# Kernel optimization log

Hardware: AMD Instinct MI355X
Metric: run time of the kernel (lower is better)

## Reference

```python
import jax, jax.numpy as jnp
import numpy as np

DIM = 128
GROUPS = [1, 2, 2, 3]


def setup_inputs() -> dict:
    key = jax.random.key(0)
    ks = jax.random.split(key, 8)
    c = DIM
    def p(k, shape, scale=0.02):
        return jax.random.normal(k, shape, dtype=jnp.float32) * scale
    return {
        "x": jax.random.normal(ks[0], (8, c, 128, 128), dtype=jnp.float32),
        "temperature": jnp.ones((4, 1, 1), dtype=jnp.float32),
        "w_qkv": p(ks[1], (3 * c, c)),            # Conv2d(dim, 3*dim, 1), bias=False
        "w_dw": p(ks[2], (3 * c, 1, 3, 3)),        # depthwise 3x3, groups=3*dim
        "w_proj": p(ks[3], (c, c)),                # Conv2d(dim, dim, 1), bias=False
        "w_gate": p(ks[4], (c, c)),                # Intra gatingConv (Conv1d k=1)
        "b_gate": jnp.zeros((c,), jnp.float32),
        "w_down": p(ks[5], (c // 2, c)),           # Intra down
        "b_down": jnp.zeros((c // 2,), jnp.float32),
        "w_up": p(ks[6], (c, c // 2)),             # Intra up
        "b_up": jnp.zeros((c,), jnp.float32),
    }


def _group_sizes(c):
    total = sum(GROUPS)
    sizes = [int(r / total * c) for r in GROUPS]
    sizes[-1] += c - sum(sizes)
    return sizes


def _forward(x, temperature, w_qkv, w_dw, w_proj, w_gate, b_gate,
             w_down, b_down, w_up, b_up):
    b, c, h, w = x.shape
    L = h * w
    # qkv = dwconv3x3(conv1x1(x))
    qkv = jnp.einsum('bchw,oc->bohw', x, w_qkv)
    qkv = jax.lax.conv_general_dilated(
        qkv, w_dw, (1, 1), 'SAME', feature_group_count=3 * c,
        dimension_numbers=('NCHW', 'OIHW', 'NCHW'))
    q, k, v = jnp.split(qkv.reshape(b, 3 * c, L), 3, axis=1)
    # ReGroup: sort channels by mean q activation (descending), split into groups
    channel_mean = q.mean(axis=(0, 2))            # (c,)
    idx = jnp.argsort(-channel_mean)
    q, k, v = q[:, idx], k[:, idx], v[:, idx]
    sizes = _group_sizes(c)
    outs, caches, cache_means = [], [], []
    start = 0
    for i, g in enumerate(sizes):
        qg = q[:, start:start + g]
        kg = k[:, start:start + g]
        vg = v[:, start:start + g]
        start += g
        qn = qg / jnp.maximum(jnp.linalg.norm(qg, axis=-1, keepdims=True), 1e-12)
        kn = kg / jnp.maximum(jnp.linalg.norm(kg, axis=-1, keepdims=True), 1e-12)
        attn = jax.nn.softmax(
            jnp.einsum('bcl,bdl->bcd', qn, kn) * temperature[i, 0, 0], axis=-1)
        outs.append(jnp.einsum('bcd,bdl->bcl', attn, vg))   # (b, g, L)
        tc = jax.lax.stop_gradient(qn + kn)                 # detached cache
        caches.append(tc)
        # per-group mean over L, channel-tiled/padded to c (for cache update)
        gm = tc.mean(axis=-1)                               # (b, g)
        rep = max(1, c // g)
        gm = jnp.tile(gm, (1, rep))
        gm = gm[:, :c] if gm.shape[1] >= c else jnp.pad(gm, ((0, 0), (0, c - gm.shape[1])))
        cache_means.append(gm)
    out_all = jnp.concatenate(outs, axis=1)       # (b, c, L)
    tmp_caches = jnp.concatenate(caches, axis=1)  # (b, c, L)
    # CalculateCurrentLayerCache: bilinear upsample of (1,1) map == broadcast
    s = int(L ** 0.5 + 0.9999)
    acc = sum(cache_means) / float(len(cache_means))        # (b, c)
    qv_cache = jnp.broadcast_to((acc * 0.9)[:, :, None, None], (b, c, s, s))
    # Intra cache modulation: gated = gelu(conv(x1+x2)) * (x1+x2); up(down(gated))
    sxy = out_all + tmp_caches
    gating = jax.nn.gelu(jnp.einsum('bcl,oc->bol', sxy, w_gate) + b_gate[:, None],
                         approximate=False)
    gated = gating * sxy
    mod = jnp.einsum('bcl,oc->bol', gated, w_down) + b_down[:, None]
    mod = jnp.einsum('bcl,oc->bol', mod, w_up) + b_up[:, None]
    out_all = mod + out_all
    out_all = jnp.einsum('bchw,oc->bohw', out_all.reshape(b, c, h, w), w_proj)
    return out_all, qv_cache


def reference(x, temperature, w_qkv, w_dw, w_proj, w_gate, b_gate,
              w_down, b_down, w_up, b_up):
    return _forward(x, temperature, w_qkv, w_dw, w_proj, w_gate, b_gate,
                    w_down, b_down, w_up, b_up)
```

## Files before the change

kernel.cpp:

```cpp
#include <hip/hip_runtime.h>
#include <math.h>

#define B_ 8
#define C_ 128
#define O3_ 384
#define H_ 128
#define W_ 128
#define L_ 16384
#define NS_ 64
#define MAXP_ 2304

typedef float f32x4 __attribute__((ext_vector_type(4)));
typedef short bf16x8 __attribute__((ext_vector_type(8)));

static __device__ __forceinline__ ushort f2bf(float f) {
    uint u = __float_as_uint(f);
    u += 0x7fffu + ((u >> 16) & 1u);
    return (ushort)(u >> 16);
}
static __device__ __forceinline__ float bf2f(ushort h) {
    return __uint_as_float(((uint)h) << 16);
}

__global__ __launch_bounds__(256) void wsplit_k(
    const float* __restrict__ wa, const float* __restrict__ wb,
    const float* __restrict__ wc, const float* __restrict__ wd,
    short* __restrict__ ha, short* __restrict__ la,
    short* __restrict__ hb, short* __restrict__ lb,
    short* __restrict__ hc, short* __restrict__ lc,
    short* __restrict__ hd, short* __restrict__ ld)
{
    const int sel = blockIdx.y;
    const float* w = sel == 0 ? wa : (sel == 1 ? wb : (sel == 2 ? wc : wd));
    short* ph = sel == 0 ? ha : (sel == 1 ? hb : (sel == 2 ? hc : hd));
    short* pl = sel == 0 ? la : (sel == 1 ? lb : (sel == 2 ? lc : ld));
    const int n = sel == 0 ? 49152 : (sel == 1 ? 16384 : 8192);
    const int i = blockIdx.x * 256 + threadIdx.x;
    if (i < n) {
        float v = w[i];
        ushort h = f2bf(v);
        ph[i] = (short)h;
        pl[i] = (short)f2bf(v - bf2f(h));
    }
}

__global__ __launch_bounds__(256) void wsplit1_k(const float* __restrict__ w,
    short* __restrict__ ph, short* __restrict__ pl, int n)
{
    const int i = blockIdx.x * 256 + threadIdx.x;
    if (i < n) {
        float v = w[i];
        ushort h = f2bf(v);
        ph[i] = (short)h;
        pl[i] = (short)f2bf(v - bf2f(h));
    }
}

__global__ __launch_bounds__(256) void transp_k(const float* __restrict__ x,
    short* __restrict__ xhi, short* __restrict__ xlo)
{
    __shared__ float t[128][33];
    const int b = blockIdx.y;
    const int l0 = blockIdx.x * 32;
    const int tid = threadIdx.x;
    {
        const int c = tid >> 1, half = tid & 1;
        const float* src = x + ((size_t)b * C_ + c) * L_ + l0 + half * 16;
#pragma unroll
        for (int u = 0; u < 4; u++) {
            float4 v = *reinterpret_cast<const float4*>(src + u * 4);
            t[c][half * 16 + u * 4 + 0] = v.x;
            t[c][half * 16 + u * 4 + 1] = v.y;
            t[c][half * 16 + u * 4 + 2] = v.z;
            t[c][half * 16 + u * 4 + 3] = v.w;
        }
    }
    __syncthreads();
    {
        const int l = tid >> 3, strip = tid & 7;
        uint hi[8], lo[8];
#pragma unroll
        for (int i = 0; i < 8; i++) {
            float a0 = t[strip * 16 + 2 * i][l], a1 = t[strip * 16 + 2 * i + 1][l];
            ushort h0 = f2bf(a0), h1 = f2bf(a1);
            ushort g0 = f2bf(a0 - bf2f(h0)), g1 = f2bf(a1 - bf2f(h1));
            hi[i] = (uint)h0 | ((uint)h1 << 16);
            lo[i] = (uint)g0 | ((uint)g1 << 16);
        }
        size_t ob = ((size_t)b * L_ + l0 + l) * C_ + strip * 16;
        uint4* ph = reinterpret_cast<uint4*>(xhi + ob);
        uint4* pl = reinterpret_cast<uint4*>(xlo + ob);
        ph[0] = *reinterpret_cast<uint4*>(&hi[0]);
        ph[1] = *reinterpret_cast<uint4*>(&hi[4]);
        pl[0] = *reinterpret_cast<uint4*>(&lo[0]);
        pl[1] = *reinterpret_cast<uint4*>(&lo[4]);
    }
}

template<int KD, int OT, int MODE>
__global__ __launch_bounds__(256) void mgemm_k(
    const short* __restrict__ Whi, const short* __restrict__ Wlo,
    const float* __restrict__ bias,
    const short* __restrict__ Ahi, const short* __restrict__ Alo,
    const float* __restrict__ E0,
    float* __restrict__ Yf, short* __restrict__ Yhi, short* __restrict__ Ylo)
{
    constexpr int WC = OT / 64;
    constexpr int WR = 4 / WC;
    constexpr int LT = WR * 64;
    constexpr int T  = KD / 32;
    constexpr int ABYTES = LT * 64;
    constexpr int BBYTES = OT * KD * 2;
    constexpr int CA = WR;
    constexpr int CB = (OT * KD) / 2048;
    __shared__ __align__(16) char sAh[ABYTES];
    __shared__ __align__(16) char sAl[ABYTES];
    __shared__ __align__(16) char sBh[BBYTES];
    __shared__ __align__(16) char sBl[BBYTES];

    const int tid = threadIdx.x;
    const int lane = tid & 63;
    const int wid = tid >> 6;
    const int wr = wid / WC, wc = wid % WC;
    const int oB = blockIdx.x * OT;
    const int lB = blockIdx.y * LT;
    const int ON = gridDim.x * OT;
    const int b  = blockIdx.z;
    const int ln15 = lane & 15, lg = lane >> 4;
    const int m0A = (ln15 >> 1) & 3;
    const int m0B = ln15 & 3;
    const int m1B = (ln15 >> 2) & (T - 1);

    const size_t abase = ((size_t)b * L_ + lB) * KD;

    {
#pragma unroll
        for (int p = 0; p < CB; p++) {
            const int id = tid + p * 256;
            const int row = id / (KD / 8), cs = id % (KD / 8);
            const int tt = cs >> 2, ks = cs & 3;
            const size_t src = (size_t)(oB + row) * KD + cs * 8;
            const int dst = row * (KD * 2) + ((tt ^ ((row >> 2) & (T - 1))) * 64)
                          + ((ks ^ (row & 3)) << 4);
            *reinterpret_cast<uint4*>(sBh + dst) = *reinterpret_cast<const uint4*>(Whi + src);
            *reinterpret_cast<uint4*>(sBl + dst) = *reinterpret_cast<const uint4*>(Wlo + src);
        }
    }

    uint4 pAh[CA], pAl[CA];
    auto ldgA = [&](int t) {
#pragma unroll
        for (int p = 0; p < CA; p++) {
            const int id = tid + p * 256;
            const int row = id >> 2, s = id & 3;
            const size_t src = abase + (size_t)row * KD + t * 32 + s * 8;
            pAh[p] = *reinterpret_cast<const uint4*>(Ahi + src);
            pAl[p] = *reinterpret_cast<const uint4*>(Alo + src);
        }
    };
    auto stA = [&]() {
#pragma unroll
        for (int p = 0; p < CA; p++) {
            const int id = tid + p * 256;
            const int row = id >> 2, s = id & 3;
            const int dst = row * 64 + ((s ^ ((row >> 1) & 3)) << 4);
            *reinterpret_cast<uint4*>(sAh + dst) = pAh[p];
            *reinterpret_cast<uint4*>(sAl + dst) = pAl[p];
        }
    };

    f32x4 acc[4][4];
#pragma unroll
    for (int m = 0; m < 4; m++)
#pragma unroll
        for (int n = 0; n < 4; n++)
#pragma unroll
            for (int r = 0; r < 4; r++) acc[m][n][r] = 0.f;

    ldgA(0);
    stA();
    __syncthreads();

    for (int t = 0; t < T; t++) {
        bf16x8 Ah[4], Al[4], Bh[4], Bl[4];
#pragma unroll
        for (int m = 0; m < 4; m++) {
            const int row = wr * 64 + m * 16 + ln15;
            const int ab = row * 64 + ((lg ^ m0A) << 4);
            Ah[m] = *reinterpret_cast<const bf16x8*>(sAh + ab);
            Al[m] = *reinterpret_cast<const bf16x8*>(sAl + ab);
        }
#pragma unroll
        for (int n = 0; n < 4; n++) {
            const int row = wc * 64 + n * 16 + ln15;
            const int bb = row * (KD * 2) + ((t ^ m1B) * 64) + ((lg ^ m0B) << 4);
            Bh[n] = *reinterpret_cast<const bf16x8*>(sBh + bb);
            Bl[n] = *reinterpret_cast<const bf16x8*>(sBl + bb);
        }
        __syncthreads();
        if (t + 1 < T) ldgA(t + 1);
#pragma unroll
        for (int n = 0; n < 4; n++)
#pragma unroll
            for (int m = 0; m < 4; m++) {
                acc[m][n] = __builtin_amdgcn_mfma_f32_16x16x32_bf16(Ah[m], Bh[n], acc[m][n], 0, 0, 0);
                acc[m][n] = __builtin_amdgcn_mfma_f32_16x16x32_bf16(Ah[m], Bl[n], acc[m][n], 0, 0, 0);
                acc[m][n] = __builtin_amdgcn_mfma_f32_16x16x32_bf16(Al[m], Bh[n], acc[m][n], 0, 0, 0);
            }
        if (t + 1 < T) { stA(); __syncthreads(); }
    }

#pragma unroll
    for (int m = 0; m < 4; m++) {
        const int l = lB + wr * 64 + m * 16 + lg * 4;
#pragma unroll
        for (int n = 0; n < 4; n++) {
            const int o = oB + wc * 64 + n * 16 + ln15;
            if constexpr (MODE == 4) {
                float4 r4 = {acc[m][n][0], acc[m][n][1], acc[m][n][2], acc[m][n][3]};
                *reinterpret_cast<float4*>(&Yf[((size_t)b * ON + o) * L_ + l]) = r4;
            } else {
                float bv = bias[o];
#pragma unroll
                for (int r = 0; r < 4; r++) {
                    size_t yi = ((size_t)b * L_ + l + r) * ON + o;
                    float a = acc[m][n][r] + bv;
                    if constexpr (MODE == 1) {
                        float sxy = bf2f((ushort)Ahi[yi]) + bf2f((ushort)Alo[yi]);
                        a = 0.5f * a * (1.f + erff(a * 0.70710678118654752f)) * sxy;
                    }
                    if constexpr (MODE == 3) a += E0[yi];
                    ushort h = f2bf(a);
                    ushort g = f2bf(a - bf2f(h));
                    Yhi[yi] = (short)h;
                    Ylo[yi] = (short)g;
                }
            }
        }
    }
}

__global__ __launch_bounds__(256) void dwconv_k(const float* __restrict__ in,
    const float* __restrict__ wdw, float* __restrict__ outp,
    float* __restrict__ sumq, float* __restrict__ sumk,
    float* __restrict__ ssq, float* __restrict__ ssk)
{
    const int ch = blockIdx.x, b = blockIdx.y;
    const int tid = threadIdx.x;
    const int tx = tid & 31, band = tid >> 5;
    const int x0 = tx * 4;
    const int y0 = band * 16;
    const size_t base = ((size_t)b * O3_ + ch) * L_;
    const float* wp = wdw + ch * 9;
    float w0 = wp[0], w1 = wp[1], w2 = wp[2], w3 = wp[3], w4 = wp[4],
          w5 = wp[5], w6 = wp[6], w7 = wp[7], w8 = wp[8];

    float s1 = 0.f, s2 = 0.f;
    float b0[6], b1[6], b2[6];

    auto loadrow = [&](int gy, float* r) {
        if ((unsigned)gy < (unsigned)H_) {
            const float* rp = in + base + (size_t)gy * W_;
            float4 m = *reinterpret_cast<const float4*>(rp + x0);
            r[0] = (x0 > 0) ? rp[x0 - 1] : 0.f;
            r[1] = m.x; r[2] = m.y; r[3] = m.z; r[4] = m.w;
            r[5] = (x0 < W_ - 4) ? rp[x0 + 4] : 0.f;
        } else {
            r[0] = r[1] = r[2] = r[3] = r[4] = r[5] = 0.f;
        }
    };
    auto conv3 = [&](const float* ra, const float* rb, const float* rc, int yy) {
        float o0 = ra[0]*w0 + ra[1]*w1 + ra[2]*w2 + rb[0]*w3 + rb[1]*w4 + rb[2]*w5 + rc[0]*w6 + rc[1]*w7 + rc[2]*w8;
        float o1 = ra[1]*w0 + ra[2]*w1 + ra[3]*w2 + rb[1]*w3 + rb[2]*w4 + rb[3]*w5 + rc[1]*w6 + rc[2]*w7 + rc[3]*w8;
        float o2 = ra[2]*w0 + ra[3]*w1 + ra[4]*w2 + rb[2]*w3 + rb[3]*w4 + rb[4]*w5 + rc[2]*w6 + rc[3]*w7 + rc[4]*w8;
        float o3 = ra[3]*w0 + ra[4]*w1 + ra[5]*w2 + rb[3]*w3 + rb[4]*w4 + rb[5]*w5 + rc[3]*w6 + rc[4]*w7 + rc[5]*w8;
        float4 o4 = {o0, o1, o2, o3};
        *reinterpret_cast<float4*>(&outp[base + (size_t)(y0 + yy) * W_ + x0]) = o4;
        s1 += (o0 + o1) + (o2 + o3);
        s2 += o0*o0 + o1*o1 + o2*o2 + o3*o3;
    };

    loadrow(y0 - 1, b0);
    loadrow(y0,     b1);
#pragma unroll
    for (int y3 = 0; y3 < 15; y3 += 3) {
        loadrow(y0 + y3 + 1, b2); conv3(b0, b1, b2, y3);
        loadrow(y0 + y3 + 2, b0); conv3(b1, b2, b0, y3 + 1);
        loadrow(y0 + y3 + 3, b1); conv3(b2, b0, b1, y3 + 2);
    }
    loadrow(y0 + 16, b2); conv3(b0, b1, b2, 15);

    __shared__ float r1[256], r2[256];
    if (ch < 256) {
        r1[tid] = s1; r2[tid] = s2;
        __syncthreads();
        for (int st = 128; st > 0; st >>= 1) {
            if (tid < st) { r1[tid] += r1[tid + st]; r2[tid] += r2[tid + st]; }
            __syncthreads();
        }
        if (tid == 0) {
            if (ch < 128) { sumq[b * 128 + ch] = r1[0]; ssq[b * 128 + ch] = r2[0]; }
            else          { sumk[b * 128 + ch - 128] = r1[0]; ssk[b * 128 + ch - 128] = r2[0]; }
        }
    }
}

__global__ void combine_k(const float* __restrict__ sumq, const float* __restrict__ sumk,
    const float* __restrict__ ssq, const float* __restrict__ ssk,
    int* __restrict__ idxp, float* __restrict__ rqc, float* __restrict__ rkc,
    float* __restrict__ gm)
{
    const int t = threadIdx.x;
    __shared__ double cms[128];
    double s = 0.0;
    for (int b = 0; b < B_; b++) s += (double)sumq[b * 128 + t];
    cms[t] = s;
    float rqv[B_], rkv[B_];
    for (int b = 0; b < B_; b++) {
        rqv[b] = 1.f / fmaxf(sqrtf(ssq[b * 128 + t]), 1e-12f);
        rkv[b] = 1.f / fmaxf(sqrtf(ssk[b * 128 + t]), 1e-12f);
        rqc[b * 128 + t] = rqv[b];
        rkc[b * 128 + t] = rkv[b];
    }
    __syncthreads();
    const double mv = cms[t];
    int r = 0;
    for (int j = 0; j < 128; j++) {
        double o = cms[j];
        if (o > mv || (o == mv && j < t)) r++;
    }
    idxp[r] = t;
    for (int b = 0; b < B_; b++)
        gm[b * 128 + r] = (rqv[b] * sumq[b * 128 + t] + rkv[b] * sumk[b * 128 + t]) * (1.0f / L_);
}

template<int G>
__global__ __launch_bounds__(256) void score_k(const float* __restrict__ dw, const int* __restrict__ idxp,
    int start, int gi, float* __restrict__ spart)
{
    constexpr int TS = G / 16;
    const int split = blockIdx.x, b = blockIdx.y;
    const int tid = threadIdx.x, tx = tid & 15, ty = tid >> 4;
    __shared__ float sQ[G][66];
    __shared__ float sK[G][66];
    __shared__ int sc[G];
    if (tid < G) sc[tid] = idxp[start + tid];
    __syncthreads();

    float acc[TS][TS];
#pragma unroll
    for (int i = 0; i < TS; i++)
#pragma unroll
        for (int j = 0; j < TS; j++) acc[i][j] = 0.f;

    const int l0 = split * (L_ / NS_);
    constexpr int LPT = (G * 64) / 256;
    for (int chk = 0; chk < L_ / NS_; chk += 64) {
#pragma unroll
        for (int i = 0; i < LPT; i++) {
            int id = tid + i * 256;
            int row = id >> 6, lc = id & 63;
            size_t base = ((size_t)b * O3_ + sc[row]) * L_ + l0 + chk + lc;
            sQ[row][lc] = dw[base];
            sK[row][lc] = dw[base + (size_t)128 * L_];
        }
        __syncthreads();
#pragma unroll
        for (int kk = 0; kk < 64; kk++) {
            float qv[TS], kv[TS];
#pragma unroll
            for (int j = 0; j < TS; j++) { qv[j] = sQ[ty * TS + j][kk]; kv[j] = sK[tx * TS + j][kk]; }
#pragma unroll
            for (int i = 0; i < TS; i++)
#pragma unroll
                for (int j = 0; j < TS; j++)
                    acc[i][j] = fmaf(qv[i], kv[j], acc[i][j]);
        }
        __syncthreads();
    }
    float* op = spart + (((size_t)(b * 4 + gi)) * NS_ + split) * MAXP_;
#pragma unroll
    for (int i = 0; i < TS; i++)
#pragma unroll
        for (int j = 0; j < TS; j++)
            op[(ty * TS + i) * G + tx * TS + j] = acc[i][j];
}

__global__ __launch_bounds__(256) void softmax_k(const float* __restrict__ spart,
    const float* __restrict__ rqc, const float* __restrict__ rkc, const int* __restrict__ idxp,
    const float* __restrict__ temp, float* __restrict__ attn)
{
    const int gi = blockIdx.x, b = blockIdx.y;
    const int g = (gi == 0) ? 16 : (gi == 3 ? 48 : 32);
    const int start = (gi == 0) ? 0 : (gi == 1 ? 16 : (gi == 2 ? 48 : 80));
    __shared__ float S[MAXP_];
    __shared__ int sidx[48];
    if (threadIdx.x < g) sidx[threadIdx.x] = idxp[start + threadIdx.x];
    __syncthreads();
    const float tv = temp[gi];
    for (int p = threadIdx.x; p < g * g; p += 256) {
        float s = 0.f;
        const float* sp = spart + ((size_t)(b * 4 + gi)) * NS_ * MAXP_ + p;
        for (int k = 0; k < NS_; k++) s += sp[(size_t)k * MAXP_];
        int cc = p / g, dd = p - cc * g;
        S[p] = s * rqc[b * 128 + sidx[cc]] * rkc[b * 128 + sidx[dd]] * tv;
    }
    __syncthreads();
    const int wv = threadIdx.x >> 6, lane = threadIdx.x & 63;
    for (int r = wv; r < g; r += 4) {
        float val = (lane < g) ? S[r * g + lane] : -1e30f;
        float mx = val;
        for (int m = 32; m > 0; m >>= 1) mx = fmaxf(mx, __shfl_xor(mx, m));
        float e = (lane < g) ? expf(val - mx) : 0.f;
        float sum = e;
        for (int m = 32; m > 0; m >>= 1) sum += __shfl_xor(sum, m);
        if (lane < g) attn[((size_t)(b * 4 + gi)) * MAXP_ + r * g + lane] = e / sum;
    }
}

template<int G>
__global__ __launch_bounds__(256) void av3_k(const float* __restrict__ dw, const int* __restrict__ idxp,
    const float* __restrict__ rqc, const float* __restrict__ rkc,
    const float* __restrict__ attn, int start, int gi,
    float* __restrict__ outallT, short* __restrict__ sxyhi, short* __restrict__ sxylo)
{
    constexpr int C4 = G / 4;
    constexpr int GP = G + 1;
    const int b = blockIdx.y;
    const int lB = blockIdx.x * 64;
    const int tid = threadIdx.x;
    __shared__ float sA[G * GP];
    __shared__ float sV[64][GP];
    __shared__ int cv[G];
    __shared__ float rqs[G], rks[G];
    if (tid < G) {
        int c0 = idxp[start + tid];
        cv[tid] = c0;
        rqs[tid] = rqc[b * 128 + c0];
        rks[tid] = rkc[b * 128 + c0];
    }
    for (int p = tid; p < G * G; p += 256) {
        int cc = p / G, dd = p - cc * G;
        sA[cc * GP + dd] = attn[((size_t)(b * 4 + gi)) * MAXP_ + p];
    }
    __syncthreads();
    for (int idx = tid; idx < 64 * G; idx += 256) {
        int l = idx & 63, d = idx >> 6;
        sV[l][d] = dw[((size_t)b * O3_ + 256 + cv[d]) * L_ + lB + l];
    }
    __syncthreads();
    const int strip = tid & 3, l = tid >> 2;
    float acc[C4];
#pragma unroll
    for (int j = 0; j < C4; j++) acc[j] = 0.f;
    for (int d = 0; d < G; d++) {
        float vd = sV[l][d];
#pragma unroll
        for (int j = 0; j < C4; j++)
            acc[j] = fmaf(sA[(strip * C4 + j) * GP + d], vd, acc[j]);
    }
    const size_t ob = ((size_t)b * L_ + lB + l) * C_ + start + strip * C4;
    float sv[C4];
#pragma unroll
    for (int j = 0; j < C4; j++) {
        int c = strip * C4 + j;
        float q = dw[((size_t)b * O3_ + cv[c]) * L_ + lB + l];
        float k = dw[((size_t)b * O3_ + 128 + cv[c]) * L_ + lB + l];
        sv[j] = acc[j] + rqs[c] * q + rks[c] * k;
    }
#pragma unroll
    for (int j = 0; j < C4; j += 4) {
        float4 o4 = {acc[j], acc[j + 1], acc[j + 2], acc[j + 3]};
        *reinterpret_cast<float4*>(&outallT[ob + j]) = o4;
    }
#pragma unroll
    for (int j = 0; j < C4; j += 2) {
        ushort h0 = f2bf(sv[j]), h1 = f2bf(sv[j + 1]);
        ushort g0 = f2bf(sv[j] - bf2f(h0)), g1 = f2bf(sv[j + 1] - bf2f(h1));
        *reinterpret_cast<uint*>(&sxyhi[ob + j]) = (uint)h0 | ((uint)h1 << 16);
        *reinterpret_cast<uint*>(&sxylo[ob + j]) = (uint)g0 | ((uint)g1 << 16);
    }
}

__global__ __launch_bounds__(256) void qvc_k(const float* __restrict__ gm, float* __restrict__ outq)
{
    const int cpos = blockIdx.x, b = blockIdx.y;
    const float* g = gm + b * 128;
    float v = g[cpos & 15] + g[16 + (cpos & 31)] + g[48 + (cpos & 31)];
    if (cpos < 96) v += g[80 + (cpos % 48)];
    v *= 0.225f;
    float4 vv = {v, v, v, v};
    float4* op = reinterpret_cast<float4*>(outq + ((size_t)b * C_ + cpos) * L_);
    for (int i = threadIdx.x; i < L_ / 4; i += 256) op[i] = vv;
}

extern "C" void kernel_launch(void* const* d_in, const int* in_sizes, int n_in,
                              void* d_out, int out_size, void* d_ws, size_t ws_size,
                              hipStream_t stream)
{
    const float* x     = (const float*)d_in[0];
    const float* temp  = (const float*)d_in[1];
    const float* wqkv  = (const float*)d_in[2];
    const float* wdw   = (const float*)d_in[3];
    const float* wproj = (const float*)d_in[4];
    const float* wgate = (const float*)d_in[5];
    const float* bgate = (const float*)d_in[6];
    const float* wdown = (const float*)d_in[7];
    const float* bdown = (const float*)d_in[8];
    const float* wup   = (const float*)d_in[9];
    const float* bup   = (const float*)d_in[10];
    float* out = (float*)d_out;
    float* ws  = (float*)d_ws;

    float* qkvCL = ws;
    float* dwCL  = ws + 50331648ull;
    short* xThi  = (short*)(ws + 50331648ull);
    short* xTlo  = xThi + 16777216ull;
    float* outallT = ws;
    short* sxyhi   = (short*)(ws + 16777216ull);
    short* sxylo   = sxyhi + 16777216ull;
    short* gatedhi = (short*)(ws + 33554432ull);
    short* gatedlo = gatedhi + 16777216ull;
    short* mod1hi  = (short*)(ws + 16777216ull);
    short* mod1lo  = mod1hi + 8388608ull;
    short* out2hi  = (short*)(ws + 33554432ull);
    short* out2lo  = out2hi + 16777216ull;
    short* wprojh  = (short*)(ws + 25165824ull);
    short* wprojl  = wprojh + 16384ull;

    float* spart = out;
    float* attn  = out + 4718592ull;
    float* sumq  = out + 4800000ull;
    float* sumk  = out + 4801024ull;
    float* ssq   = out + 4802048ull;
    float* ssk   = out + 4803072ull;
    float* rqc   = out + 4804096ull;
    float* rkc   = out + 4805120ull;
    float* gm    = out + 4806144ull;
    int*   idxp  = (int*)(out + 4807168ull);
    short* wqkvh = (short*)(out + 4900000ull);
    short* wqkvl = (short*)(out + 4924576ull);
    short* wgateh= (short*)(out + 4949152ull);
    short* wgatel= (short*)(out + 4957344ull);
    short* wdownh= (short*)(out + 4965536ull);
    short* wdownl= (short*)(out + 4969632ull);
    short* wuph  = (short*)(out + 4973728ull);
    short* wupl  = (short*)(out + 4977824ull);

    wsplit_k<<<dim3(192, 4), 256, 0, stream>>>(wqkv, wgate, wdown, wup,
        wqkvh, wqkvl, wgateh, wgatel, wdownh, wdownl, wuph, wupl);
    transp_k<<<dim3(512, 8), 256, 0, stream>>>(x, xThi, xTlo);
    mgemm_k<128, 128, 4><<<dim3(3, 128, 8), 256, 0, stream>>>(
        wqkvh, wqkvl, nullptr, xThi, xTlo, nullptr, qkvCL, nullptr, nullptr);
    dwconv_k<<<dim3(384, 8), 256, 0, stream>>>(qkvCL, wdw, dwCL, sumq, sumk, ssq, ssk);
    combine_k<<<1, 128, 0, stream>>>(sumq, sumk, ssq, ssk, idxp, rqc, rkc, gm);
    score_k<16><<<dim3(NS_, 8), 256, 0, stream>>>(dwCL, idxp, 0, 0, spart);
    score_k<32><<<dim3(NS_, 8), 256, 0, stream>>>(dwCL, idxp, 16, 1, spart);
    score_k<32><<<dim3(NS_, 8), 256, 0, stream>>>(dwCL, idxp, 48, 2, spart);
    score_k<48><<<dim3(NS_, 8), 256, 0, stream>>>(dwCL, idxp, 80, 3, spart);
    softmax_k<<<dim3(4, 8), 256, 0, stream>>>(spart, rqc, rkc, idxp, temp, attn);
    av3_k<16><<<dim3(256, 8), 256, 0, stream>>>(dwCL, idxp, rqc, rkc, attn, 0, 0, outallT, sxyhi, sxylo);
    av3_k<32><<<dim3(256, 8), 256, 0, stream>>>(dwCL, idxp, rqc, rkc, attn, 16, 1, outallT, sxyhi, sxylo);
    av3_k<32><<<dim3(256, 8), 256, 0, stream>>>(dwCL, idxp, rqc, rkc, attn, 48, 2, outallT, sxyhi, sxylo);
    av3_k<48><<<dim3(256, 8), 256, 0, stream>>>(dwCL, idxp, rqc, rkc, attn, 80, 3, outallT, sxyhi, sxylo);
    mgemm_k<128, 128, 1><<<dim3(1, 128, 8), 256, 0, stream>>>(
        wgateh, wgatel, bgate, sxyhi, sxylo, nullptr, nullptr, gatedhi, gatedlo);
    qvc_k<<<dim3(128, 8), 256, 0, stream>>>(gm, out + 16777216ull);
    mgemm_k<128, 64, 2><<<dim3(1, 64, 8), 256, 0, stream>>>(
        wdownh, wdownl, bdown, gatedhi, gatedlo, nullptr, nullptr, mod1hi, mod1lo);
    mgemm_k<64, 128, 3><<<dim3(1, 128, 8), 256, 0, stream>>>(
        wuph, wupl, bup, mod1hi, mod1lo, outallT, nullptr, out2hi, out2lo);
    wsplit1_k<<<64, 256, 0, stream>>>(wproj, wprojh, wprojl, 16384);
    mgemm_k<128, 128, 4><<<dim3(1, 128, 8), 256, 0, stream>>>(
        wprojh, wprojl, nullptr, out2hi, out2lo, nullptr, out, nullptr, nullptr);
}
```

Baseline: 766.2 us.

## Load GEMM A-operand fragments directly from global into registers, double-buffered

The bf16-split GEMM kernel no longer stages the activation (A) tile through shared memory. Each lane now loads its MFMA A fragments straight from global memory into two register buffers, prefetching two k-steps ahead, and the per-iteration barriers are removed. This cuts LDS traffic and synchronisation in exchange for more registers and less coalesced global loads, since each lane reads 16-byte chunks across rows. Rows shared by the wave columns (wc) are now fetched redundantly from global memory instead of once per block.

```diff
diff --git a/kernel.cpp b/kernel.cpp
--- a/kernel.cpp
+++ b/kernel.cpp
@@ -109,12 +109,8 @@
     constexpr int WR = 4 / WC;
     constexpr int LT = WR * 64;
     constexpr int T  = KD / 32;
-    constexpr int ABYTES = LT * 64;
     constexpr int BBYTES = OT * KD * 2;
-    constexpr int CA = WR;
     constexpr int CB = (OT * KD) / 2048;
-    __shared__ __align__(16) char sAh[ABYTES];
-    __shared__ __align__(16) char sAl[ABYTES];
     __shared__ __align__(16) char sBh[BBYTES];
     __shared__ __align__(16) char sBl[BBYTES];
 
@@ -127,69 +123,48 @@
     const int ON = gridDim.x * OT;
     const int b  = blockIdx.z;
     const int ln15 = lane & 15, lg = lane >> 4;
-    const int m0A = (ln15 >> 1) & 3;
     const int m0B = ln15 & 3;
     const int m1B = (ln15 >> 2) & (T - 1);
 
-    const size_t abase = ((size_t)b * L_ + lB) * KD;
-
-    {
-#pragma unroll
-        for (int p = 0; p < CB; p++) {
-            const int id = tid + p * 256;
-            const int row = id / (KD / 8), cs = id % (KD / 8);
-            const int tt = cs >> 2, ks = cs & 3;
-            const size_t src = (size_t)(oB + row) * KD + cs * 8;
-            const int dst = row * (KD * 2) + ((tt ^ ((row >> 2) & (T - 1))) * 64)
-                          + ((ks ^ (row & 3)) << 4);
-            *reinterpret_cast<uint4*>(sBh + dst) = *reinterpret_cast<const uint4*>(Whi + src);
-            *reinterpret_cast<uint4*>(sBl + dst) = *reinterpret_cast<const uint4*>(Wlo + src);
-        }
-    }
-
-    uint4 pAh[CA], pAl[CA];
-    auto ldgA = [&](int t) {
-#pragma unroll
-        for (int p = 0; p < CA; p++) {
-            const int id = tid + p * 256;
-            const int row = id >> 2, s = id & 3;
-            const size_t src = abase + (size_t)row * KD + t * 32 + s * 8;
-            pAh[p] = *reinterpret_cast<const uint4*>(Ahi + src);
-            pAl[p] = *reinterpret_cast<const uint4*>(Alo + src);
+#pragma unroll
+    for (int p = 0; p < CB; p++) {
+        const int id = tid + p * 256;
+        const int row = id / (KD / 8), cs = id % (KD / 8);
+        const int tt = cs >> 2, ks = cs & 3;
+        const size_t src = (size_t)(oB + row) * KD + cs * 8;
+        const int dst = row * (KD * 2) + ((tt ^ ((row >> 2) & (T - 1))) * 64)
+                      + ((ks ^ (row & 3)) << 4);
+        *reinterpret_cast<uint4*>(sBh + dst) = *reinterpret_cast<const uint4*>(Whi + src);
+        *reinterpret_cast<uint4*>(sBl + dst) = *reinterpret_cast<const uint4*>(Wlo + src);
+    }
+
+    f32x4 acc[4][4];
+#pragma unroll
+    for (int m = 0; m < 4; m++)
+#pragma unroll
+        for (int n = 0; n < 4; n++)
+#pragma unroll
+            for (int r = 0; r < 4; r++) acc[m][n][r] = 0.f;
+
+    const size_t arow = ((size_t)b * L_ + lB + wr * 64 + ln15) * KD + lg * 8;
+
+    bf16x8 A0h[4], A0l[4], A1h[4], A1l[4];
+    auto ldA = [&](bf16x8* Ah, bf16x8* Al, int t) {
+#pragma unroll
+        for (int m = 0; m < 4; m++) {
+            const size_t g = arow + (size_t)(m * 16) * KD + t * 32;
+            Ah[m] = *reinterpret_cast<const bf16x8*>(Ahi + g);
+            Al[m] = *reinterpret_cast<const bf16x8*>(Alo + g);
         }
     };
-    auto stA = [&]() {
-#pragma unroll
-        for (int p = 0; p < CA; p++) {
-            const int id = tid + p * 256;
-            const int row = id >> 2, s = id & 3;
-            const int dst = row * 64 + ((s ^ ((row >> 1) & 3)) << 4);
-            *reinterpret_cast<uint4*>(sAh + dst) = pAh[p];
-            *reinterpret_cast<uint4*>(sAl + dst) = pAl[p];
-        }
-    };
-
-    f32x4 acc[4][4];
-#pragma unroll
-    for (int m = 0; m < 4; m++)
-#pragma unroll
-        for (int n = 0; n < 4; n++)
-#pragma unroll
-            for (int r = 0; r < 4; r++) acc[m][n][r] = 0.f;
-
-    ldgA(0);
-    stA();
-    __syncthreads();
-
+
+    ldA(A0h, A0l, 0);
+    if (T > 1) ldA(A1h, A1l, 1);
+    __syncthreads();
+
+#pragma unroll
     for (int t = 0; t < T; t++) {
-        bf16x8 Ah[4], Al[4], Bh[4], Bl[4];
-#pragma unroll
-        for (int m = 0; m < 4; m++) {
-            const int row = wr * 64 + m * 16 + ln15;
-            const int ab = row * 64 + ((lg ^ m0A) << 4);
-            Ah[m] = *reinterpret_cast<const bf16x8*>(sAh + ab);
-            Al[m] = *reinterpret_cast<const bf16x8*>(sAl + ab);
-        }
+        bf16x8 Bh[4], Bl[4];
 #pragma unroll
         for (int n = 0; n < 4; n++) {
             const int row = wc * 64 + n * 16 + ln15;
@@ -197,8 +172,8 @@
             Bh[n] = *reinterpret_cast<const bf16x8*>(sBh + bb);
             Bl[n] = *reinterpret_cast<const bf16x8*>(sBl + bb);
         }
-        __syncthreads();
-        if (t + 1 < T) ldgA(t + 1);
+        const bf16x8* Ah = (t & 1) ? A1h : A0h;
+        const bf16x8* Al = (t & 1) ? A1l : A0l;
 #pragma unroll
         for (int n = 0; n < 4; n++)
 #pragma unroll
@@ -207,7 +182,10 @@
                 acc[m][n] = __builtin_amdgcn_mfma_f32_16x16x32_bf16(Ah[m], Bl[n], acc[m][n], 0, 0, 0);
                 acc[m][n] = __builtin_amdgcn_mfma_f32_16x16x32_bf16(Al[m], Bh[n], acc[m][n], 0, 0, 0);
             }
-        if (t + 1 < T) { stA(); __syncthreads(); }
+        if (t + 2 < T) {
+            if (t & 1) ldA(A1h, A1l, t + 2);
+            else       ldA(A0h, A0l, t + 2);
+        }
     }
 
 #pragma unroll
```

Measured after the change: 721.6 us. -5.8%, faster.
